# Kernel tuning notes

Measured on AMD Instinct MI355X. Metric: run time of the kernel, lower is better.

Reference implementation:

```python
import jax, jax.numpy as jnp
import numpy as np

B, L, D_MODEL = 2, 4096, 768
D_STATE, D_CONV, EXPAND = 16, 4, 2
D_INNER = EXPAND * D_MODEL
DT_RANK = -(-D_MODEL // 16)  # ceil(d_model/16) = 48


def _silu(x):
    return x * jax.nn.sigmoid(x)


def _dwconv(x, w, b):
    # x: (B, D_INNER, L); w: (D_INNER, K). Causal depthwise conv (torch pads both
    # sides with K-1 then slices [:L] == left-pad K-1, right-pad 0).
    y = jax.lax.conv_general_dilated(
        x, w[:, None, :], window_strides=(1,), padding=[(w.shape[-1] - 1, 0)],
        dimension_numbers=('NCH', 'OIH', 'NCH'), feature_group_count=x.shape[1])
    return y + b[None, :, None]


def _selective_scan(u, delta, A, Bm, Cm, Dv):
    # u, delta: (b,d,L); A: (d,n); Bm, Cm: (b,n,L); Dv: (d,)
    uT = jnp.moveaxis(u, -1, 0)      # (L,b,d)
    dT = jnp.moveaxis(delta, -1, 0)  # (L,b,d)
    BT = jnp.moveaxis(Bm, -1, 0)     # (L,b,n)
    CT = jnp.moveaxis(Cm, -1, 0)     # (L,b,n)

    def step(h, inp):
        u_t, d_t, B_t, C_t = inp
        dA = jnp.exp(d_t[..., None] * A)                       # (b,d,n)
        h = dA * h + (d_t * u_t)[..., None] * B_t[:, None, :]  # (b,d,n)
        y = jnp.einsum('bdn,bn->bd', h, C_t)
        return h, y

    h0 = jnp.zeros((u.shape[0], A.shape[0], A.shape[1]), u.dtype)
    _, ys = jax.lax.scan(step, h0, (uT, dT, BT, CT))
    y = jnp.moveaxis(ys, 0, -1)  # (b,d,L)
    return y + u * Dv[None, :, None]


def _branch(x, z, conv_w, conv_b, xproj_w, dtproj_w, dt_bias, A_log, Dv):
    x = _silu(_dwconv(x, conv_w, conv_b))
    dbl = jnp.einsum('bdl,ed->bel', x, xproj_w)  # e = DT_RANK + 2*D_STATE
    dt_low = dbl[:, :DT_RANK]
    Bm = dbl[:, DT_RANK:DT_RANK + D_STATE]
    Cm = dbl[:, DT_RANK + D_STATE:]
    dt = jnp.einsum('brl,dr->bdl', dt_low, dtproj_w)
    delta = jax.nn.softplus(dt + dt_bias[None, :, None])
    A = -jnp.exp(A_log)
    y = _selective_scan(x, delta, A, Bm, Cm, Dv)
    return y * _silu(z)


def _forward(hidden_states, in_proj_w, out_proj_w, conv_w_a, conv_b_a, conv_w_b,
             conv_b_b, x_proj_a_w, x_proj_b_w, dt_proj_a_w, dt_proj_b_w,
             dt_bias_a, dt_bias_b, A_a_log, A_b_log, D_a, D_b):
    xz = jnp.einsum('bld,ed->bel', hidden_states, in_proj_w)  # (B, 2*D_INNER, L)
    x_a, z_a = xz[:, :D_INNER], xz[:, D_INNER:]
    y_a = _branch(x_a, z_a, conv_w_a, conv_b_a, x_proj_a_w, dt_proj_a_w,
                  dt_bias_a, A_a_log, D_a)
    xz_b = xz[:, :, ::-1]  # flip sequence for backward direction
    x_b, z_b = xz_b[:, :D_INNER], xz_b[:, D_INNER:]
    y_b = _branch(x_b, z_b, conv_w_b, conv_b_b, x_proj_b_w, dt_proj_b_w,
                  dt_bias_b, A_b_log, D_b)
    y = y_a + y_b[:, :, ::-1]
    return jnp.einsum('bdl,od->blo', y, out_proj_w)  # (B, L, D_MODEL)


def setup_inputs() -> dict:
    key = jax.random.key(0)
    ks = jax.random.split(key, 10)
    s = 0.02
    rng = np.random.default_rng(0)
    # dt bias init: inverse-softplus of dt ~ LogUniform(1e-3, 1e-1)
    dt = np.exp(rng.uniform(size=D_INNER) * (np.log(0.1) - np.log(0.001))
                + np.log(0.001)).clip(min=1e-4)
    inv_dt = (dt + np.log(-np.expm1(-dt))).astype(np.float32)
    A_log = np.log(np.tile(np.arange(1, D_STATE + 1, dtype=np.float32),
                           (D_INNER, 1)))
    return {
        'hidden_states': jax.random.normal(ks[0], (B, L, D_MODEL), jnp.float32),
        'in_proj_w': s * jax.random.normal(ks[1], (2 * D_INNER, D_MODEL), jnp.float32),
        'out_proj_w': s * jax.random.normal(ks[2], (D_MODEL, D_INNER), jnp.float32),
        'conv_w_a': s * jax.random.normal(ks[3], (D_INNER, D_CONV), jnp.float32),
        'conv_b_a': jnp.zeros((D_INNER,), jnp.float32),
        'conv_w_b': s * jax.random.normal(ks[4], (D_INNER, D_CONV), jnp.float32),
        'conv_b_b': jnp.zeros((D_INNER,), jnp.float32),
        'x_proj_a_w': s * jax.random.normal(ks[5], (DT_RANK + 2 * D_STATE, D_INNER), jnp.float32),
        'x_proj_b_w': s * jax.random.normal(ks[6], (DT_RANK + 2 * D_STATE, D_INNER), jnp.float32),
        'dt_proj_a_w': (DT_RANK ** -0.5) * jax.random.uniform(ks[7], (D_INNER, DT_RANK), jnp.float32, -1.0, 1.0),
        'dt_proj_b_w': (DT_RANK ** -0.5) * jax.random.uniform(ks[8], (D_INNER, DT_RANK), jnp.float32, -1.0, 1.0),
        'dt_bias_a': jnp.asarray(inv_dt),
        'dt_bias_b': jnp.asarray(inv_dt),
        'A_a_log': jnp.asarray(A_log),
        'A_b_log': jnp.asarray(A_log),
        'D_a': jnp.ones((D_INNER,), jnp.float32),
        'D_b': jnp.ones((D_INNER,), jnp.float32),
    }


def reference(hidden_states, in_proj_w, out_proj_w, conv_w_a, conv_b_a, conv_w_b,
              conv_b_b, x_proj_a_w, x_proj_b_w, dt_proj_a_w, dt_proj_b_w,
              dt_bias_a, dt_bias_b, A_a_log, A_b_log, D_a, D_b):
    return _forward(hidden_states, in_proj_w, out_proj_w, conv_w_a, conv_b_a,
                    conv_w_b, conv_b_b, x_proj_a_w, x_proj_b_w, dt_proj_a_w,
                    dt_proj_b_w, dt_bias_a, dt_bias_b, A_a_log, A_b_log, D_a, D_b)
```

## Files before the change

kernel.cpp:

```cpp
#include <hip/hip_runtime.h>
#include <math.h>

#define BQ 2
#define LQ 4096
#define DM 768
#define DI 1536
#define DS 16
#define E80 80
#define NC 32
#define CH 128

typedef _Float16 half8 __attribute__((ext_vector_type(8)));
typedef _Float16 half4v __attribute__((ext_vector_type(4)));
typedef float f32x4 __attribute__((ext_vector_type(4)));

__device__ __forceinline__ ushort f2h_bits(float x) {
    return __builtin_bit_cast(ushort, (_Float16)x);
}

#define GLDS16(gsrc, ldst)                                                  \
    __builtin_amdgcn_global_load_lds(                                       \
        (const __attribute__((address_space(1))) void*)(gsrc),              \
        (__attribute__((address_space(3))) void*)(ldst), 16, 0, 0)

__global__ __launch_bounds__(256)
void pack_fp16(const float* __restrict__ src, _Float16* __restrict__ dst)
{
    long i = ((long)blockIdx.x * 256 + threadIdx.x) * 4;
    float4 v = *(const float4*)(src + i);
    half4v o = {(_Float16)v.x, (_Float16)v.y, (_Float16)v.z, (_Float16)v.w};
    *(half4v*)(dst + i) = o;
}

__global__ __launch_bounds__(256)
void pack_dtw(const float* __restrict__ dwa, const float* __restrict__ dwb,
              _Float16* __restrict__ dtw)
{
    int idx = blockIdx.x * 256 + threadIdx.x;
    int br = idx / DI, d = idx % DI;
    const float* W = (br ? dwb : dwa) + (long)d * 48;
    _Float16* o = dtw + (long)idx * 64;
#pragma unroll
    for (int k = 0; k < 48; k++) o[k] = (_Float16)W[k];
#pragma unroll
    for (int k = 48; k < 64; k++) o[k] = (_Float16)0.f;
}

template <typename CT>
__global__ __launch_bounds__(256)
void gemm_mfma(const _Float16* __restrict__ Ah, const _Float16* __restrict__ Bh,
               CT* __restrict__ C, int K, int ldA, int ldB, int ldC,
               long strideA, long strideB, long strideC)
{
    __shared__ uint4 Af[16][64];
    __shared__ uint4 Bf[16][64];
    const int bz = blockIdx.z;
    const _Float16* Ab = Ah + (long)bz * strideA;
    const _Float16* Bb = Bh + (long)bz * strideB;
    CT* Cb = C + (long)bz * strideC;
    const int m0 = blockIdx.y * 128, n0 = blockIdx.x * 128;
    const int tid = threadIdx.x, w = tid >> 6, lane = tid & 63;
    const int mh = w & 1, nh = w >> 1;

    const _Float16* asrc[4];
    const _Float16* bsrc[4];
#pragma unroll
    for (int i = 0; i < 4; i++) {
        int f = w * 4 + i;
        int ks = f >> 3, t = f & 7;
        asrc[i] = Ab + (long)(m0 + t * 16 + (lane & 15)) * ldA + ks * 32 + (lane >> 4) * 8;
        bsrc[i] = Bb + (long)(n0 + t * 16 + (lane & 15)) * ldB + ks * 32 + (lane >> 4) * 8;
    }

    f32x4 acc[4][4];
#pragma unroll
    for (int i = 0; i < 4; i++)
#pragma unroll
        for (int j = 0; j < 4; j++) acc[i][j] = {0.f, 0.f, 0.f, 0.f};

    for (int k0 = 0; k0 < K; k0 += 64) {
#pragma unroll
        for (int i = 0; i < 4; i++) {
            GLDS16(asrc[i], &Af[w * 4 + i][0]);
            GLDS16(bsrc[i], &Bf[w * 4 + i][0]);
            asrc[i] += 64; bsrc[i] += 64;
        }
        __syncthreads();
#pragma unroll
        for (int ks = 0; ks < 2; ks++) {
            uint4 au[4], bu[4];
#pragma unroll
            for (int i = 0; i < 4; i++) {
                au[i] = Af[ks * 8 + mh * 4 + i][lane];
                bu[i] = Bf[ks * 8 + nh * 4 + i][lane];
            }
#pragma unroll
            for (int i = 0; i < 4; i++) {
                half8 av = __builtin_bit_cast(half8, au[i]);
#pragma unroll
                for (int j = 0; j < 4; j++) {
                    half8 bv = __builtin_bit_cast(half8, bu[j]);
                    acc[i][j] = __builtin_amdgcn_mfma_f32_16x16x32_f16(
                        av, bv, acc[i][j], 0, 0, 0);
                }
            }
        }
        __syncthreads();
    }
    const int r0 = (lane >> 4) * 4, cn = lane & 15;
#pragma unroll
    for (int i = 0; i < 4; i++) {
        int mrow = m0 + (mh * 4 + i) * 16 + r0;
#pragma unroll
        for (int j = 0; j < 4; j++) {
            int col = n0 + (nh * 4 + j) * 16 + cn;
#pragma unroll
            for (int r = 0; r < 4; r++)
                Cb[(long)(mrow + r) * ldC + col] = (CT)acc[i][j][r];
        }
    }
}

__global__ __launch_bounds__(256)
void conv_silu_t(const _Float16* __restrict__ xz,
                 const float* __restrict__ cwa, const float* __restrict__ cba,
                 const float* __restrict__ cwb, const float* __restrict__ cbb,
                 _Float16* __restrict__ ut)
{
    __shared__ float lraw[64][67];
    __shared__ float cu[64][72];
    __shared__ float lcw[64][5];
    const int l0 = blockIdx.x * 64, d0 = blockIdx.y * 64;
    const int z = blockIdx.z;
    const int br = z >> 1, b = z & 1;
    const _Float16* xb = xz + ((long)b * 2 * DI + d0) * LQ;
    const float* CW = br ? cwb : cwa;
    const float* CB = br ? cbb : cba;
    const int tid = threadIdx.x;

    {
        int dd = tid >> 2, k = tid & 3;
        lcw[dd][k] = CW[(d0 + dd) * 4 + k];
        if (tid < 64) lcw[tid][4] = CB[d0 + tid];
    }
    for (int i = tid; i < 64 * 67; i += 256) {
        int dd = i / 67, cc = i % 67;
        int src = l0 - 3 + cc;
        float v = 0.f;
        if (src >= 0)
            v = (float)xb[(long)dd * LQ + (br ? (LQ - 1 - src) : src)];
        lraw[dd][cc] = v;
    }
    __syncthreads();
#pragma unroll
    for (int q = 0; q < 16; q++) {
        int o = tid + q * 256;
        int dd = o & 63, ll = o >> 6;
        float a = lcw[dd][4];
        a = fmaf(lraw[dd][ll + 0], lcw[dd][0], a);
        a = fmaf(lraw[dd][ll + 1], lcw[dd][1], a);
        a = fmaf(lraw[dd][ll + 2], lcw[dd][2], a);
        a = fmaf(lraw[dd][ll + 3], lcw[dd][3], a);
        cu[ll][dd] = a * (1.f / (1.f + __expf(-a)));
    }
    __syncthreads();
    const int dg = (tid & 7) * 8;
#pragma unroll
    for (int p = 0; p < 2; p++) {
        int ll = (tid >> 3) + p * 32;
        float4 v0 = *(const float4*)&cu[ll][dg];
        float4 v1 = *(const float4*)&cu[ll][dg + 4];
        uint4 o;
        o.x = f2h_bits(v0.x) | ((unsigned)f2h_bits(v0.y) << 16);
        o.y = f2h_bits(v0.z) | ((unsigned)f2h_bits(v0.w) << 16);
        o.z = f2h_bits(v1.x) | ((unsigned)f2h_bits(v1.y) << 16);
        o.w = f2h_bits(v1.z) | ((unsigned)f2h_bits(v1.w) << 16);
        *(uint4*)(ut + ((long)z * LQ + l0 + ll) * DI + d0 + dg) = o;
    }
}

__global__ __launch_bounds__(256)
void xproj_mfma(const _Float16* __restrict__ ut, const _Float16* __restrict__ xpw,
                float* __restrict__ dbl)
{
    __shared__ uint4 Af[8][64];
    __shared__ uint4 Bf[10][64];
    const int m0 = blockIdx.x * 64;
    const int z = blockIdx.y;
    const _Float16* A = ut + (long)z * LQ * DI;
    const _Float16* W = xpw + (long)(z >> 1) * E80 * DI;
    float* out = dbl + (long)z * LQ * E80;
    const int tid = threadIdx.x, w = tid >> 6, lane = tid & 63;

    f32x4 acc[5];
#pragma unroll
    for (int j = 0; j < 5; j++) acc[j] = {0.f, 0.f, 0.f, 0.f};

    for (int k0 = 0; k0 < DI; k0 += 64) {
#pragma unroll
        for (int i = 0; i < 2; i++) {
            int f = w + i * 4;
            int row = m0 + (f & 3) * 16 + (lane & 15);
            int koff = k0 + (f >> 2) * 32 + (lane >> 4) * 8;
            Af[f][lane] = *(const uint4*)(A + (long)row * DI + koff);
        }
        for (int i = tid; i < 640; i += 256) {
            int f = i >> 6, ln = i & 63;
            int e = (f >> 1) * 16 + (ln & 15);
            int koff = k0 + (f & 1) * 32 + (ln >> 4) * 8;
            Bf[f][ln] = *(const uint4*)(W + (long)e * DI + koff);
        }
        __syncthreads();
#pragma unroll
        for (int ks = 0; ks < 2; ks++) {
            half8 av = __builtin_bit_cast(half8, Af[ks * 4 + w][lane]);
#pragma unroll
            for (int j = 0; j < 5; j++) {
                half8 bv = __builtin_bit_cast(half8, Bf[j * 2 + ks][lane]);
                acc[j] = __builtin_amdgcn_mfma_f32_16x16x32_f16(av, bv, acc[j], 0, 0, 0);
            }
        }
        __syncthreads();
    }
    const int r0 = (lane >> 4) * 4, cn = lane & 15;
    const int row = m0 + w * 16 + r0;
#pragma unroll
    for (int j = 0; j < 5; j++)
#pragma unroll
        for (int r = 0; r < 4; r++)
            out[(long)(row + r) * E80 + j * 16 + cn] = acc[j][r];
}

__global__ __launch_bounds__(256)
void delta_mfma(const float* __restrict__ dbl, const _Float16* __restrict__ dtw,
                const float* __restrict__ dba, const float* __restrict__ dbb,
                _Float16* __restrict__ dlt)
{
    __shared__ uint4 Af[8][64];
    __shared__ uint4 Bf[16][64];
    const int m0 = blockIdx.x * 64;
    const int n0 = blockIdx.y * 128;
    const int z  = blockIdx.z;
    const float* bias = (z >> 1) ? dbb : dba;
    const float* Ab = dbl + (long)z * LQ * E80;
    const _Float16* Wb = dtw + (long)(z >> 1) * DI * 64;
    _Float16* ob = dlt + (long)z * LQ * DI;
    const int tid = threadIdx.x, w = tid >> 6, lane = tid & 63;

#pragma unroll
    for (int i = 0; i < 2; i++) {
        int s = tid + i * 256;
        int f = s >> 6, ln = s & 63;
        int mt = f >> 1, ks = f & 1;
        int row = m0 + mt * 16 + (ln & 15);
        int koff = ks * 32 + (ln >> 4) * 8;
        uint4 o = {0u, 0u, 0u, 0u};
        if (koff < 48) {
            const float* p = Ab + (long)row * E80 + koff;
            float4 v0 = *(const float4*)p;
            float4 v1 = *(const float4*)(p + 4);
            o.x = f2h_bits(v0.x) | ((unsigned)f2h_bits(v0.y) << 16);
            o.y = f2h_bits(v0.z) | ((unsigned)f2h_bits(v0.w) << 16);
            o.z = f2h_bits(v1.x) | ((unsigned)f2h_bits(v1.y) << 16);
            o.w = f2h_bits(v1.z) | ((unsigned)f2h_bits(v1.w) << 16);
        }
        Af[f][ln] = o;
    }
#pragma unroll
    for (int i = 0; i < 4; i++) {
        int s = tid + i * 256;
        int f = s >> 6, ln = s & 63;
        int nt = f >> 1, ks = f & 1;
        int d = n0 + nt * 16 + (ln & 15);
        int koff = ks * 32 + (ln >> 4) * 8;
        Bf[f][ln] = *(const uint4*)(Wb + (long)d * 64 + koff);
    }
    __syncthreads();

    f32x4 acc[8];
#pragma unroll
    for (int j = 0; j < 8; j++) acc[j] = {0.f, 0.f, 0.f, 0.f};
#pragma unroll
    for (int ks = 0; ks < 2; ks++) {
        half8 av = __builtin_bit_cast(half8, Af[w * 2 + ks][lane]);
#pragma unroll
        for (int j = 0; j < 8; j++) {
            half8 bv = __builtin_bit_cast(half8, Bf[j * 2 + ks][lane]);
            acc[j] = __builtin_amdgcn_mfma_f32_16x16x32_f16(av, bv, acc[j], 0, 0, 0);
        }
    }
    const int r0 = (lane >> 4) * 4, cn = lane & 15;
    const int row = m0 + w * 16 + r0;
#pragma unroll
    for (int j = 0; j < 8; j++) {
        int d = n0 + j * 16 + cn;
        float bi = bias[d];
#pragma unroll
        for (int r = 0; r < 4; r++) {
            float a = acc[j][r] + bi;
            float sp = (a > 20.f) ? a : __logf(1.f + __expf(a));
            ob[(long)(row + r) * DI + d] = (_Float16)sp;
        }
    }
}

__global__ __launch_bounds__(256)
void transpose_z(const _Float16* __restrict__ xz, _Float16* __restrict__ zt)
{
    __shared__ float t[64][65];
    const int l0 = blockIdx.x * 64, d0 = blockIdx.y * 64, b = blockIdx.z;
    const _Float16* src = xz + ((long)b * 2 * DI + DI + d0) * LQ + l0;
    const int tid = threadIdx.x;
#pragma unroll
    for (int p = 0; p < 2; p++) {
        int g = tid + p * 256;
        int dd = g >> 3, c8 = (g & 7) * 8;
        half8 v = *(const half8*)&src[(long)dd * LQ + c8];
#pragma unroll
        for (int j = 0; j < 8; j++) t[c8 + j][dd] = (float)v[j];
    }
    __syncthreads();
    const int l = tid >> 2, seg = (tid & 3) * 16;
    ushort tmp[16];
#pragma unroll
    for (int j = 0; j < 16; j++) tmp[j] = f2h_bits(t[l][seg + j]);
    uint4 p0, p1;
    p0.x = tmp[0] | (tmp[1] << 16);  p0.y = tmp[2] | (tmp[3] << 16);
    p0.z = tmp[4] | (tmp[5] << 16);  p0.w = tmp[6] | (tmp[7] << 16);
    p1.x = tmp[8] | (tmp[9] << 16);  p1.y = tmp[10] | (tmp[11] << 16);
    p1.z = tmp[12] | (tmp[13] << 16); p1.w = tmp[14] | (tmp[15] << 16);
    ushort* dst = (ushort*)(zt + ((long)b * LQ + l0 + l) * DI + d0 + seg);
    *(uint4*)dst = p0;
    *(uint4*)(dst + 8) = p1;
}

__global__ __launch_bounds__(256)
void scan_p1(const _Float16* __restrict__ ut, const _Float16* __restrict__ dlt,
             const float* __restrict__ dbl,
             const float* __restrict__ Ala, const float* __restrict__ Alb,
             float* __restrict__ Sdl, float* __restrict__ Hloc)
{
    const int d = blockIdx.x * 256 + threadIdx.x;
    const int c = blockIdx.y;
    const int z = blockIdx.z;
    const int br = z >> 1;
    const float* Al = br ? Alb : Ala;
    float An[16];
#pragma unroll
    for (int i = 0; i < 4; i++) {
        float4 v = *(const float4*)&Al[(long)d * 16 + i * 4];
        An[i * 4] = -__expf(v.x); An[i * 4 + 1] = -__expf(v.y);
        An[i * 4 + 2] = -__expf(v.z); An[i * 4 + 3] = -__expf(v.w);
    }
    bool fast = true;
#pragma unroll
    for (int n = 0; n < 16; n++)
        fast = fast && (__builtin_fabsf(An[n] + (float)(n + 1)) < 1e-3f);

    const long lbase = (long)z * LQ + (long)c * CH;
    const _Float16* ub = ut + lbase * DI + d;
    const _Float16* db = dlt + lbase * DI + d;
    const float* bc = dbl + lbase * E80 + 48;

    float h[16];
#pragma unroll
    for (int n = 0; n < 16; n++) h[n] = 0.f;
    float sdl = 0.f;

    for (int t0 = 0; t0 < CH; t0 += 8) {
        _Float16 uu[8], dd[8];
#pragma unroll
        for (int j = 0; j < 8; j++) {
            uu[j] = ub[(long)(t0 + j) * DI];
            dd[j] = db[(long)(t0 + j) * DI];
        }
#pragma unroll
        for (int j = 0; j < 8; j++) {
            float dl = (float)dd[j];
            float u  = (float)uu[j];
            sdl += dl;
            float du = dl * u;
            const float* Bp = bc + (long)(t0 + j) * E80;
            float Bv[16];
#pragma unroll
            for (int i = 0; i < 4; i++) {
                float4 v = *(const float4*)&Bp[i * 4];
                Bv[i * 4] = v.x; Bv[i * 4 + 1] = v.y;
                Bv[i * 4 + 2] = v.z; Bv[i * 4 + 3] = v.w;
            }
            if (fast) {
                float r = __expf(-dl);
                float p = r;
                h[0] = fmaf(p, h[0], du * Bv[0]);
#pragma unroll
                for (int n = 1; n < 16; n++) {
                    p *= r;
                    h[n] = fmaf(p, h[n], du * Bv[n]);
                }
            } else {
#pragma unroll
                for (int n = 0; n < 16; n++)
                    h[n] = fmaf(__expf(dl * An[n]), h[n], du * Bv[n]);
            }
        }
    }
    Sdl[((long)z * NC + c) * DI + d] = sdl;
    float* Hp = Hloc + (((long)z * NC + c) * DI + d) * 16;
#pragma unroll
    for (int i = 0; i < 4; i++)
        *(float4*)&Hp[i * 4] = make_float4(h[i * 4], h[i * 4 + 1], h[i * 4 + 2], h[i * 4 + 3]);
}

__global__ __launch_bounds__(256)
void scan_p2(const float* __restrict__ Sdl, const float* __restrict__ Hloc,
             const float* __restrict__ Ala, const float* __restrict__ Alb,
             float* __restrict__ h0)
{
    const int idx = blockIdx.x * 256 + threadIdx.x;
    const int z = blockIdx.y;
    const int d = idx >> 4, n = idx & 15;
    const float* Al = (z >> 1) ? Alb : Ala;
    const float An = -__expf(Al[(long)d * 16 + n]);
    float h = 0.f;
    for (int c = 0; c < NC; c++) {
        h0[((long)z * NC + c) * DI * 16 + idx] = h;
        float sdl = Sdl[((long)z * NC + c) * DI + d];
        float Hl = Hloc[((long)z * NC + c) * DI * 16 + idx];
        h = fmaf(__expf(An * sdl), h, Hl);
    }
}

__global__ __launch_bounds__(256)
void scan_p3(const _Float16* __restrict__ ut, const _Float16* __restrict__ dlt,
             const float* __restrict__ dbl, const float* __restrict__ h0,
             const float* __restrict__ Ala, const float* __restrict__ Alb,
             const float* __restrict__ Da, const float* __restrict__ Db,
             _Float16* __restrict__ ya, _Float16* __restrict__ yb)
{
    const int d = blockIdx.x * 256 + threadIdx.x;
    const int c = blockIdx.y;
    const int z = blockIdx.z;
    const int br = z >> 1, b = z & 1;
    const float* Al = br ? Alb : Ala;
    float An[16];
#pragma unroll
    for (int i = 0; i < 4; i++) {
        float4 v = *(const float4*)&Al[(long)d * 16 + i * 4];
        An[i * 4] = -__expf(v.x); An[i * 4 + 1] = -__expf(v.y);
        An[i * 4 + 2] = -__expf(v.z); An[i * 4 + 3] = -__expf(v.w);
    }
    bool fast = true;
#pragma unroll
    for (int n = 0; n < 16; n++)
        fast = fast && (__builtin_fabsf(An[n] + (float)(n + 1)) < 1e-3f);

    const float Dd = (br ? Db : Da)[d];
    const long lbase = (long)z * LQ + (long)c * CH;
    const _Float16* ub = ut + lbase * DI + d;
    const _Float16* db = dlt + lbase * DI + d;
    const float* bc = dbl + lbase * E80 + 48;
    const float* Hp = h0 + (((long)z * NC + c) * DI + d) * 16;
    float h[16];
#pragma unroll
    for (int i = 0; i < 4; i++) {
        float4 v = *(const float4*)&Hp[i * 4];
        h[i * 4] = v.x; h[i * 4 + 1] = v.y; h[i * 4 + 2] = v.z; h[i * 4 + 3] = v.w;
    }
    _Float16* yo = br ? yb : ya;

    for (int t0 = 0; t0 < CH; t0 += 8) {
        _Float16 uu[8], dd[8];
#pragma unroll
        for (int j = 0; j < 8; j++) {
            uu[j] = ub[(long)(t0 + j) * DI];
            dd[j] = db[(long)(t0 + j) * DI];
        }
#pragma unroll
        for (int j = 0; j < 8; j++) {
            float dl = (float)dd[j];
            float u  = (float)uu[j];
            float du = dl * u;
            const float* Bp = bc + (long)(t0 + j) * E80;
            float Bv[16], Cv[16];
#pragma unroll
            for (int i = 0; i < 4; i++) {
                float4 v = *(const float4*)&Bp[i * 4];
                Bv[i * 4] = v.x; Bv[i * 4 + 1] = v.y;
                Bv[i * 4 + 2] = v.z; Bv[i * 4 + 3] = v.w;
                float4 w2 = *(const float4*)&Bp[16 + i * 4];
                Cv[i * 4] = w2.x; Cv[i * 4 + 1] = w2.y;
                Cv[i * 4 + 2] = w2.z; Cv[i * 4 + 3] = w2.w;
            }
            float y = u * Dd;
            if (fast) {
                float r = __expf(-dl);
                float p = r;
                h[0] = fmaf(p, h[0], du * Bv[0]);
                y = fmaf(h[0], Cv[0], y);
#pragma unroll
                for (int n = 1; n < 16; n++) {
                    p *= r;
                    h[n] = fmaf(p, h[n], du * Bv[n]);
                    y = fmaf(h[n], Cv[n], y);
                }
            } else {
#pragma unroll
                for (int n = 0; n < 16; n++) {
                    h[n] = fmaf(__expf(dl * An[n]), h[n], du * Bv[n]);
                    y = fmaf(h[n], Cv[n], y);
                }
            }
            int t = c * CH + t0 + j;
            long lorig = br ? (LQ - 1 - t) : t;
            yo[((long)b * LQ + lorig) * DI + d] = (_Float16)y;
        }
    }
}

__global__ __launch_bounds__(256)
void fuse_y(const _Float16* __restrict__ ya, const _Float16* __restrict__ yb,
            const _Float16* __restrict__ zt, _Float16* __restrict__ yf)
{
    long i = ((long)blockIdx.x * 256 + threadIdx.x) * 8;
    half8 a = *(const half8*)(ya + i);
    half8 b = *(const half8*)(yb + i);
    half8 zz = *(const half8*)(zt + i);
    half8 o;
#pragma unroll
    for (int j = 0; j < 8; j++) {
        float y = (float)a[j] + (float)b[j];
        float zv = (float)zz[j];
        o[j] = (_Float16)(y * (zv / (1.f + __expf(-zv))));
    }
    *(half8*)(yf + i) = o;
}

extern "C" void kernel_launch(void* const* d_in, const int* in_sizes, int n_in,
                              void* d_out, int out_size, void* d_ws, size_t ws_size,
                              hipStream_t stream)
{
    const float* hs  = (const float*)d_in[0];
    const float* Wi  = (const float*)d_in[1];
    const float* Wo  = (const float*)d_in[2];
    const float* cwa = (const float*)d_in[3];
    const float* cba = (const float*)d_in[4];
    const float* cwb = (const float*)d_in[5];
    const float* cbb = (const float*)d_in[6];
    const float* xpa = (const float*)d_in[7];
    const float* xpb = (const float*)d_in[8];
    const float* dwa = (const float*)d_in[9];
    const float* dwb = (const float*)d_in[10];
    const float* dba = (const float*)d_in[11];
    const float* dbb = (const float*)d_in[12];
    const float* Ala = (const float*)d_in[13];
    const float* Alb = (const float*)d_in[14];
    const float* Da  = (const float*)d_in[15];
    const float* Db  = (const float*)d_in[16];
    float* out = (float*)d_out;

    float* ws = (float*)d_ws;
    _Float16* xz   = (_Float16*)ws;
    _Float16* dl_t = (_Float16*)ws;
    _Float16* ya   = (_Float16*)(ws + 12582912);
    _Float16* yb   = (_Float16*)(ws + 18874368);
    float*    dbl  = ws + 25165824;
    _Float16* u_t  = (_Float16*)(ws + 26476544);
    _Float16* yf   = (_Float16*)(ws + 26476544);
    _Float16* z_t  = (_Float16*)(ws + 39059456);
    float*    Sdl  = ws + 45350912;
    float*    Hloc = ws + 45547520;
    float*    h0   = ws + 48693248;
    _Float16* hsb  = (_Float16*)(ws + 45350912);
    _Float16* Wib  = (_Float16*)(ws + 48496640);
    _Float16* xpw  = (_Float16*)(ws + 49676288);
    _Float16* dtw  = (_Float16*)(ws + 49799168);
    _Float16* Wob  = (_Float16*)(ws + 45350912);

    pack_fp16<<<6144, 256, 0, stream>>>(hs, hsb);
    pack_fp16<<<2304, 256, 0, stream>>>(Wi, Wib);
    pack_fp16<<<120, 256, 0, stream>>>(xpa, xpw);
    pack_fp16<<<120, 256, 0, stream>>>(xpb, xpw + 122880);
    pack_dtw<<<12, 256, 0, stream>>>(dwa, dwb, dtw);
    gemm_mfma<_Float16><<<dim3(32, 24, 2), 256, 0, stream>>>(
        Wib, hsb, xz, DM, DM, DM, LQ,
        0L, (long)LQ * DM, (long)2 * DI * LQ);
    conv_silu_t<<<dim3(64, 24, 4), 256, 0, stream>>>(xz, cwa, cba, cwb, cbb, u_t);
    xproj_mfma<<<dim3(64, 4), 256, 0, stream>>>(u_t, xpw, dbl);
    transpose_z<<<dim3(64, 24, 2), 256, 0, stream>>>(xz, z_t);
    delta_mfma<<<dim3(64, 12, 4), 256, 0, stream>>>(dbl, dtw, dba, dbb, dl_t);
    scan_p1<<<dim3(6, NC, 4), 256, 0, stream>>>(u_t, dl_t, dbl, Ala, Alb, Sdl, Hloc);
    scan_p2<<<dim3(96, 4), 256, 0, stream>>>(Sdl, Hloc, Ala, Alb, h0);
    scan_p3<<<dim3(6, NC, 4), 256, 0, stream>>>(u_t, dl_t, dbl, h0, Ala, Alb, Da, Db, ya, yb);
    pack_fp16<<<1152, 256, 0, stream>>>(Wo, Wob);
    fuse_y<<<6144, 256, 0, stream>>>(ya, yb, z_t, yf);
    gemm_mfma<float><<<dim3(6, 32, 2), 256, 0, stream>>>(
        yf, Wob, out, DI, DI, DI, DM,
        (long)LQ * DI, 0L, (long)LQ * DM);
}
```

Measured before the change: 549.6 us.

## Double-buffer LDS tiles in MFMA GEMM to overlap loads with compute

```diff
diff --git a/kernel.cpp b/kernel.cpp
--- a/kernel.cpp
+++ b/kernel.cpp
@@ -47,13 +47,13 @@
 }
 
 template <typename CT>
-__global__ __launch_bounds__(256)
+__global__ __launch_bounds__(256, 4)
 void gemm_mfma(const _Float16* __restrict__ Ah, const _Float16* __restrict__ Bh,
                CT* __restrict__ C, int K, int ldA, int ldB, int ldC,
                long strideA, long strideB, long strideC)
 {
-    __shared__ uint4 Af[16][64];
-    __shared__ uint4 Bf[16][64];
+    __shared__ uint4 Af[2][16][64];
+    __shared__ uint4 Bf[2][16][64];
     const int bz = blockIdx.z;
     const _Float16* Ab = Ah + (long)bz * strideA;
     const _Float16* Bb = Bh + (long)bz * strideB;
@@ -78,25 +78,36 @@
 #pragma unroll
         for (int j = 0; j < 4; j++) acc[i][j] = {0.f, 0.f, 0.f, 0.f};
 
-    for (int k0 = 0; k0 < K; k0 += 64) {
-#pragma unroll
-        for (int i = 0; i < 4; i++) {
-            GLDS16(asrc[i], &Af[w * 4 + i][0]);
-            GLDS16(bsrc[i], &Bf[w * 4 + i][0]);
-            asrc[i] += 64; bsrc[i] += 64;
-        }
-        __syncthreads();
+    const int nt = K >> 6;
+
+#pragma unroll
+    for (int i = 0; i < 4; i++) {
+        GLDS16(asrc[i], &Af[0][w * 4 + i][0]);
+        GLDS16(bsrc[i], &Bf[0][w * 4 + i][0]);
+        asrc[i] += 64; bsrc[i] += 64;
+    }
+    __syncthreads();
+
+    int cur = 0;
+    for (int t = 0; t < nt; ++t) {
+        if (t + 1 < nt) {
+#pragma unroll
+            for (int i = 0; i < 4; i++) {
+                GLDS16(asrc[i], &Af[cur ^ 1][w * 4 + i][0]);
+                GLDS16(bsrc[i], &Bf[cur ^ 1][w * 4 + i][0]);
+                asrc[i] += 64; bsrc[i] += 64;
+            }
+        }
 #pragma unroll
         for (int ks = 0; ks < 2; ks++) {
-            uint4 au[4], bu[4];
+            uint4 bu[4];
+#pragma unroll
+            for (int j = 0; j < 4; j++)
+                bu[j] = Bf[cur][ks * 8 + nh * 4 + j][lane];
 #pragma unroll
             for (int i = 0; i < 4; i++) {
-                au[i] = Af[ks * 8 + mh * 4 + i][lane];
-                bu[i] = Bf[ks * 8 + nh * 4 + i][lane];
-            }
-#pragma unroll
-            for (int i = 0; i < 4; i++) {
-                half8 av = __builtin_bit_cast(half8, au[i]);
+                uint4 au = Af[cur][ks * 8 + mh * 4 + i][lane];
+                half8 av = __builtin_bit_cast(half8, au);
 #pragma unroll
                 for (int j = 0; j < 4; j++) {
                     half8 bv = __builtin_bit_cast(half8, bu[j]);
@@ -106,7 +117,9 @@
             }
         }
         __syncthreads();
-    }
+        cur ^= 1;
+    }
+
     const int r0 = (lane >> 4) * 4, cn = lane & 15;
 #pragma unroll
     for (int i = 0; i < 4; i++) {
```

Result: no change. 546.9 us, median of 2 (-0.5%).

## Enlarge GEMM tiles to 256x256 with 512 threads and double-buffered LDS

Applied to the files above, without the earlier changes.

```diff
diff --git a/kernel.cpp b/kernel.cpp
--- a/kernel.cpp
+++ b/kernel.cpp
@@ -47,73 +47,84 @@
 }
 
 template <typename CT>
-__global__ __launch_bounds__(256)
+__global__ __launch_bounds__(512)
 void gemm_mfma(const _Float16* __restrict__ Ah, const _Float16* __restrict__ Bh,
                CT* __restrict__ C, int K, int ldA, int ldB, int ldC,
                long strideA, long strideB, long strideC)
 {
-    __shared__ uint4 Af[16][64];
-    __shared__ uint4 Bf[16][64];
+    __shared__ uint4 FA[2][16][64];
+    __shared__ uint4 FB[2][16][64];
     const int bz = blockIdx.z;
     const _Float16* Ab = Ah + (long)bz * strideA;
     const _Float16* Bb = Bh + (long)bz * strideB;
     CT* Cb = C + (long)bz * strideC;
-    const int m0 = blockIdx.y * 128, n0 = blockIdx.x * 128;
+    const int m0 = blockIdx.y * 256, n0 = blockIdx.x * 256;
     const int tid = threadIdx.x, w = tid >> 6, lane = tid & 63;
-    const int mh = w & 1, nh = w >> 1;
-
-    const _Float16* asrc[4];
-    const _Float16* bsrc[4];
-#pragma unroll
-    for (int i = 0; i < 4; i++) {
-        int f = w * 4 + i;
-        int ks = f >> 3, t = f & 7;
-        asrc[i] = Ab + (long)(m0 + t * 16 + (lane & 15)) * ldA + ks * 32 + (lane >> 4) * 8;
-        bsrc[i] = Bb + (long)(n0 + t * 16 + (lane & 15)) * ldB + ks * 32 + (lane >> 4) * 8;
-    }
-
-    f32x4 acc[4][4];
-#pragma unroll
-    for (int i = 0; i < 4; i++)
+    const int wr = w >> 2, wc = w & 3;
+
+    const _Float16* asrc[2];
+    const _Float16* bsrc[2];
+#pragma unroll
+    for (int i = 0; i < 2; i++) {
+        int t = w * 2 + i;
+        asrc[i] = Ab + (long)(m0 + t * 16 + (lane & 15)) * ldA + (lane >> 4) * 8;
+        bsrc[i] = Bb + (long)(n0 + t * 16 + (lane & 15)) * ldB + (lane >> 4) * 8;
+    }
+
+    f32x4 acc[8][4];
+#pragma unroll
+    for (int i = 0; i < 8; i++)
 #pragma unroll
         for (int j = 0; j < 4; j++) acc[i][j] = {0.f, 0.f, 0.f, 0.f};
 
-    for (int k0 = 0; k0 < K; k0 += 64) {
-#pragma unroll
-        for (int i = 0; i < 4; i++) {
-            GLDS16(asrc[i], &Af[w * 4 + i][0]);
-            GLDS16(bsrc[i], &Bf[w * 4 + i][0]);
-            asrc[i] += 64; bsrc[i] += 64;
-        }
-        __syncthreads();
-#pragma unroll
-        for (int ks = 0; ks < 2; ks++) {
-            uint4 au[4], bu[4];
-#pragma unroll
-            for (int i = 0; i < 4; i++) {
-                au[i] = Af[ks * 8 + mh * 4 + i][lane];
-                bu[i] = Bf[ks * 8 + nh * 4 + i][lane];
-            }
-#pragma unroll
-            for (int i = 0; i < 4; i++) {
-                half8 av = __builtin_bit_cast(half8, au[i]);
-#pragma unroll
-                for (int j = 0; j < 4; j++) {
-                    half8 bv = __builtin_bit_cast(half8, bu[j]);
-                    acc[i][j] = __builtin_amdgcn_mfma_f32_16x16x32_f16(
-                        av, bv, acc[i][j], 0, 0, 0);
-                }
-            }
-        }
-        __syncthreads();
-    }
+    const int nt = K >> 5;
+
+#define STAGE_T(dbuf)                                                       \
+    {                                                                       \
+        _Pragma("unroll")                                                   \
+        for (int i_ = 0; i_ < 2; i_++) {                                    \
+            GLDS16(asrc[i_], &FA[dbuf][w * 2 + i_][0]);                     \
+            GLDS16(bsrc[i_], &FB[dbuf][w * 2 + i_][0]);                     \
+            asrc[i_] += 32; bsrc[i_] += 32;                                 \
+        }                                                                   \
+    }
+
+    STAGE_T(0)
+    if (nt > 1) STAGE_T(1)
+
+    for (int t = 0; t < nt; ++t) {
+        const int cur = t & 1;
+        if (t + 1 < nt)
+            asm volatile("s_waitcnt vmcnt(4)" ::: "memory");
+        else
+            asm volatile("s_waitcnt vmcnt(0)" ::: "memory");
+        __builtin_amdgcn_s_barrier();
+
+        uint4 bu[4];
+#pragma unroll
+        for (int j = 0; j < 4; j++)
+            bu[j] = FB[cur][wc * 4 + j][lane];
+#pragma unroll
+        for (int i = 0; i < 8; i++) {
+            half8 av = __builtin_bit_cast(half8, FA[cur][wr * 8 + i][lane]);
+#pragma unroll
+            for (int j = 0; j < 4; j++)
+                acc[i][j] = __builtin_amdgcn_mfma_f32_16x16x32_f16(
+                    av, __builtin_bit_cast(half8, bu[j]), acc[i][j], 0, 0, 0);
+        }
+        __builtin_amdgcn_s_barrier();
+
+        if (t + 2 < nt) STAGE_T(cur)
+    }
+#undef STAGE_T
+
     const int r0 = (lane >> 4) * 4, cn = lane & 15;
 #pragma unroll
-    for (int i = 0; i < 4; i++) {
-        int mrow = m0 + (mh * 4 + i) * 16 + r0;
+    for (int i = 0; i < 8; i++) {
+        int mrow = m0 + wr * 128 + i * 16 + r0;
 #pragma unroll
         for (int j = 0; j < 4; j++) {
-            int col = n0 + (nh * 4 + j) * 16 + cn;
+            int col = n0 + wc * 64 + j * 16 + cn;
 #pragma unroll
             for (int r = 0; r < 4; r++)
                 Cb[(long)(mrow + r) * ldC + col] = (CT)acc[i][j][r];
@@ -581,7 +592,7 @@
     pack_fp16<<<120, 256, 0, stream>>>(xpa, xpw);
     pack_fp16<<<120, 256, 0, stream>>>(xpb, xpw + 122880);
     pack_dtw<<<12, 256, 0, stream>>>(dwa, dwb, dtw);
-    gemm_mfma<_Float16><<<dim3(32, 24, 2), 256, 0, stream>>>(
+    gemm_mfma<_Float16><<<dim3(16, 12, 2), 512, 0, stream>>>(
         Wib, hsb, xz, DM, DM, DM, LQ,
         0L, (long)LQ * DM, (long)2 * DI * LQ);
     conv_silu_t<<<dim3(64, 24, 4), 256, 0, stream>>>(xz, cwa, cba, cwb, cbb, u_t);
@@ -593,7 +604,7 @@
     scan_p3<<<dim3(6, NC, 4), 256, 0, stream>>>(u_t, dl_t, dbl, h0, Ala, Alb, Da, Db, ya, yb);
     pack_fp16<<<1152, 256, 0, stream>>>(Wo, Wob);
     fuse_y<<<6144, 256, 0, stream>>>(ya, yb, z_t, yf);
-    gemm_mfma<float><<<dim3(6, 32, 2), 256, 0, stream>>>(
+    gemm_mfma<float><<<dim3(3, 16, 2), 512, 0, stream>>>(
         yf, Wob, out, DI, DI, DI, DM,
         (long)LQ * DI, 0L, (long)LQ * DM);
 }
```

Result: slower. 582.9 us (+6.1%).
